# Kernel optimization log

Hardware: AMD Instinct MI355X
Metric: run time of the kernel (lower is better)

The kernel has to match this reference:

```python
import jax, jax.numpy as jnp
import numpy as np
from jax import lax

N = 1024          # proposals per image
C = 32            # num classes (incl. background at index 0)
FEAT = 4096       # box-head feature dim
NDIM = 3          # voxel boxes, zyxzyx
SCORE_THRESH = 0.05
NMS_THR = 0.5
PER_CLS_TOPN = 300
DET_PER_IMG = 100
W_CTR = jnp.array([10.0, 10.0, 10.0])
W_SIZE = jnp.array([5.0, 5.0, 5.0])
BBOX_XFORM_CLIP = float(np.log(1000.0 / 16.0))
IMG_SIZE = jnp.array([96.0, 320.0, 320.0])


def decode_boxes(reg, boxes):
    # reg: [N, C, 6] (dz,dy,dx,dsz,dsy,dsx); boxes: [N, 6] zyxzyx, TO_REMOVE=1 convention
    sizes = boxes[:, 3:] - boxes[:, :3] + 1.0            # [N,3]
    ctrs = boxes[:, :3] + 0.5 * sizes                    # [N,3]
    d_ctr = reg[..., :3] / W_CTR                         # [N,C,3]
    d_size = jnp.minimum(reg[..., 3:] / W_SIZE, BBOX_XFORM_CLIP)
    pred_ctr = d_ctr * sizes[:, None, :] + ctrs[:, None, :]
    pred_size = jnp.exp(d_size) * sizes[:, None, :]
    mins = pred_ctr - 0.5 * pred_size
    maxs = pred_ctr + 0.5 * pred_size - 1.0
    return jnp.concatenate([mins, maxs], axis=-1)        # [N,C,6]


def iou3d(b):
    # b: [M,6] zyxzyx -> [M,M] IoU (volume with +1 convention)
    lt = jnp.maximum(b[:, None, :3], b[None, :, :3])
    rb = jnp.minimum(b[:, None, 3:], b[None, :, 3:])
    whd = jnp.clip(rb - lt + 1.0, 0.0)
    inter = whd.prod(-1)
    vol = jnp.clip(b[:, 3:] - b[:, :3] + 1.0, 0.0).prod(-1)
    return inter / (vol[:, None] + vol[None, :] - inter + 1e-12)


def per_class_nms(boxes_j, scores_j):
    # boxes_j: [N,6], scores_j: [N] (softmax probs for one foreground class)
    valid = scores_j > SCORE_THRESH
    s = jnp.where(valid, scores_j, -1.0)
    order = jnp.argsort(-s)                # sorted indices (score desc), padded at end
    sb = boxes_j[order]
    ss = s[order]
    sv = valid[order]
    M = iou3d(sb)
    idx = jnp.arange(N)

    def body(i, keep):
        sup = (M[i] > NMS_THR) & (idx > i) & keep[i] & sv[i]
        return keep & ~sup

    keep = lax.fori_loop(0, N, body, sv)
    keep = keep & sv
    rank = jnp.cumsum(keep.astype(jnp.int32)) - 1
    keep = keep & (rank < PER_CLS_TOPN)
    return sb, jnp.where(keep, ss, -1.0), order, keep


def _forward(features, class_logits, box_regression, proposal_boxes):
    probs = jax.nn.softmax(class_logits, axis=-1)        # [N,C]
    reg = box_regression.reshape(N, C, 2 * NDIM)
    boxes = decode_boxes(reg, proposal_boxes)            # [N,C,6]
    # clip_to_image (remove_empty=False)
    lim = IMG_SIZE - 1.0
    boxes = jnp.concatenate([jnp.clip(boxes[..., :3], 0.0, lim),
                             jnp.clip(boxes[..., 3:], 0.0, lim)], axis=-1)
    cls_boxes = jnp.swapaxes(boxes, 0, 1)[1:]            # [C-1,N,6] skip background
    cls_scores = probs.T[1:]                             # [C-1,N]
    sb, ss, order, keep = jax.vmap(per_class_nms)(cls_boxes, cls_scores)
    all_scores = ss.reshape(-1)                          # [(C-1)*N], -1 where dropped
    all_boxes = sb.reshape(-1, 2 * NDIM)
    all_orig = order.reshape(-1)
    all_labels = jnp.broadcast_to(jnp.arange(1, C)[:, None], (C - 1, N)).reshape(-1)
    # global sort by score desc, keep top detections_per_img
    top_s, top_i = lax.top_k(all_scores, DET_PER_IMG)
    valid = top_s > 0.0
    orig = all_orig[top_i]                               # original proposal index
    feats = jnp.where(valid[:, None], features[orig], 0.0)
    pboxes = jnp.where(valid[:, None], all_boxes[top_i], 0.0)
    pscores = jnp.where(valid, top_s, 0.0)
    plabels = jnp.where(valid, all_labels[top_i], 0)
    return feats, pboxes, pscores, plabels, valid


def setup_inputs() -> dict:
    key = jax.random.key(0)
    k1, k2, k3, k4, k5 = jax.random.split(key, 5)
    features = jax.random.normal(k1, (N, FEAT), dtype=jnp.float32)
    class_logits = 2.0 * jax.random.normal(k2, (N, C), dtype=jnp.float32)
    box_regression = jax.random.normal(k3, (N, C * 2 * NDIM), dtype=jnp.float32)
    img = np.array([96.0, 320.0, 320.0], dtype=np.float32)
    mins = jax.random.uniform(k4, (N, NDIM), dtype=jnp.float32) * (img * 0.75)
    ext = jax.random.uniform(k5, (N, NDIM), dtype=jnp.float32) * (img * 0.25) + 1.0
    proposal_boxes = jnp.concatenate([mins, mins + ext - 1.0], axis=-1)
    return {"features": features, "class_logits": class_logits,
            "box_regression": box_regression, "proposal_boxes": proposal_boxes}


def reference(features, class_logits, box_regression, proposal_boxes):
    return _forward(features, class_logits, box_regression, proposal_boxes)
```

## Files before the change

kernel.cpp:

```cpp
#include <hip/hip_runtime.h>
#include <math.h>

#define NPROP 1024
#define NCLS 32
#define FEATD 4096
#define SCORE_THRESH 0.05f
#define NMS_THR 0.5f
#define DET_PER_IMG 100
#define CLS_STRIDE 128
#define BBOX_CLIP 4.135166556742356f

__device__ __forceinline__ unsigned long long u64max(unsigned long long a,
                                                     unsigned long long b) {
    return a > b ? a : b;
}

__device__ __forceinline__ unsigned flip_f32(float f) {
    unsigned u = __float_as_uint(f);
    return u ^ ((unsigned)(((int)u) >> 31) | 0x80000000u);
}
__device__ __forceinline__ float unflip_f32(unsigned u) {
    u = (u & 0x80000000u) ? (u ^ 0x80000000u) : ~u;
    return __uint_as_float(u);
}

__device__ __forceinline__ unsigned long long shfl_xor_u64(unsigned long long v,
                                                           int mask) {
    return (unsigned long long)__shfl_xor((long long)v, mask);
}

__device__ __forceinline__ void decode_box(const float* __restrict__ prop,
                                           const float* __restrict__ reg,
                                           int n, int cls, float b[6]) {
    const float lim[3] = {95.0f, 319.0f, 319.0f};
    const float* r6 = reg + n * (NCLS * 6) + cls * 6;
#pragma unroll
    for (int d = 0; d < 3; ++d) {
        float lo = prop[n * 6 + d];
        float hi = prop[n * 6 + 3 + d];
        float sz = __fadd_rn(__fsub_rn(hi, lo), 1.0f);
        float ct = __fadd_rn(lo, __fmul_rn(0.5f, sz));
        float dc = r6[d] / 10.0f;
        float ds = fminf(r6[3 + d] / 5.0f, BBOX_CLIP);
        float pc = __fadd_rn(__fmul_rn(dc, sz), ct);
        float ps = __fmul_rn(expf(ds), sz);
        float hps = __fmul_rn(0.5f, ps);
        float mn = __fsub_rn(pc, hps);
        float mx = __fsub_rn(__fadd_rn(pc, hps), 1.0f);
        b[d]     = fminf(fmaxf(mn, 0.0f), lim[d]);
        b[3 + d] = fminf(fmaxf(mx, 0.0f), lim[d]);
    }
}

__global__ __launch_bounds__(1024) void nms_kernel(const float* __restrict__ logits,
                                                   const float* __restrict__ reg,
                                                   const float* __restrict__ prop,
                                                   float* __restrict__ scores_c,
                                                   int* __restrict__ orig_c,
                                                   int* __restrict__ counts) {
    const int cls = blockIdx.x + 1;
    const int tid = threadIdx.x;
    const int lane = tid & 63, wid = tid >> 6;

    __shared__ unsigned long long kbuf[2][NPROP];
    __shared__ float sb[NPROP][6];
    __shared__ float vols[NPROP];
    __shared__ unsigned long long keepw[16];
    __shared__ int   wtot[16];
    __shared__ int   kept_cum[2];

    const float* lrow = logits + tid * NCLS;
    float4 q[8];
#pragma unroll
    for (int r = 0; r < 8; ++r) q[r] = ((const float4*)lrow)[r];
    float m = -1e30f;
#pragma unroll
    for (int r = 0; r < 8; ++r)
        m = fmaxf(m, fmaxf(fmaxf(q[r].x, q[r].y), fmaxf(q[r].z, q[r].w)));
    float ssum = 0.0f;
#pragma unroll
    for (int r = 0; r < 8; ++r) {
        ssum += expf(q[r].x - m);
        ssum += expf(q[r].y - m);
        ssum += expf(q[r].z - m);
        ssum += expf(q[r].w - m);
    }
    float xc = lrow[cls];
    float p = expf(xc - m) / ssum;
    float sv0 = (p > SCORE_THRESH) ? p : -1.0f;

    unsigned long long key =
        ((unsigned long long)flip_f32(sv0) << 32) | (unsigned)~tid;
    int pb = 0;
    for (int k = 2; k <= NPROP; k <<= 1) {
        for (int j = k >> 1; j > 0; j >>= 1) {
            unsigned long long pk;
            if (j >= 64) {
                kbuf[pb][tid] = key;
                __syncthreads();
                pk = kbuf[pb][tid ^ j];
                pb ^= 1;
            } else {
                pk = shfl_xor_u64(key, j);
            }
            bool lower = (tid & j) == 0;
            bool desc  = (tid & k) == 0;
            bool want_max = (lower == desc);
            bool pk_gt = pk > key;
            key = (want_max == pk_gt) ? pk : key;
        }
    }
    float sv = unflip_f32((unsigned)(key >> 32));
    int o = (int)(~(unsigned)key);

    float myb[6];
    decode_box(prop, reg, o, cls, myb);
#pragma unroll
    for (int d = 0; d < 6; ++d) sb[tid][d] = myb[d];
    float myvol = 1.0f;
#pragma unroll
    for (int d = 0; d < 3; ++d)
        myvol *= fmaxf(myb[3 + d] - myb[d] + 1.0f, 0.0f);
    vols[tid] = myvol;

    int mykeep = (sv > SCORE_THRESH) ? 1 : 0;
    unsigned long long m0 = __ballot(mykeep);
    if (lane == 0) keepw[wid] = m0;
    if (tid == 0) { kept_cum[0] = 0; kept_cum[1] = 0; }
    __syncthreads();

    for (int w = 0; w < 16; ++w) {
        if (kept_cum[w & 1] >= DET_PER_IMG) break;
        unsigned long long wk = 0;
        if (wid >= w) {
            wk = keepw[w];
            const int base = w << 6;
            if (wk) {
                float w0 = sb[base + lane][0], w1 = sb[base + lane][1];
                float w2 = sb[base + lane][2], w3 = sb[base + lane][3];
                float w4 = sb[base + lane][4], w5 = sb[base + lane][5];
                float wv = vols[base + lane];
                unsigned long long rest = wk;
                while (rest) {
                    int b = __ffsll((long long)rest) - 1;
                    rest &= rest - 1;
                    float b0 = sb[base + b][0], b1 = sb[base + b][1];
                    float b2 = sb[base + b][2], b3 = sb[base + b][3];
                    float b4 = sb[base + b][4], b5 = sb[base + b][5];
                    float bv = vols[base + b];
                    bool sup = false;
                    if (lane > b && ((wk >> lane) & 1)) {
                        float i0 = fmaxf(fminf(w3, b3) - fmaxf(w0, b0) + 1.0f, 0.0f);
                        float i1 = fmaxf(fminf(w4, b4) - fmaxf(w1, b1) + 1.0f, 0.0f);
                        float i2 = fmaxf(fminf(w5, b5) - fmaxf(w2, b2) + 1.0f, 0.0f);
                        float inter = i0 * i1 * i2;
                        sup = inter / (bv + wv - inter + 1e-12f) > NMS_THR;
                    }
                    unsigned long long supm = __ballot(sup);
                    wk &= ~supm;
                    rest &= ~supm;
                }
                if (wid == w) {
                    mykeep = (int)((wk >> lane) & 1);
                } else if (mykeep) {
                    unsigned long long t = wk;
                    while (t) {
                        int bb = __ffsll((long long)t) - 1;
                        t &= t - 1;
                        float b0 = sb[base + bb][0], b1 = sb[base + bb][1];
                        float b2 = sb[base + bb][2], b3 = sb[base + bb][3];
                        float b4 = sb[base + bb][4], b5 = sb[base + bb][5];
                        float bv = vols[base + bb];
                        float i0 = fmaxf(fminf(myb[3], b3) - fmaxf(myb[0], b0) + 1.0f, 0.0f);
                        float i1 = fmaxf(fminf(myb[4], b4) - fmaxf(myb[1], b1) + 1.0f, 0.0f);
                        float i2 = fmaxf(fminf(myb[5], b5) - fmaxf(myb[2], b2) + 1.0f, 0.0f);
                        float inter = i0 * i1 * i2;
                        if (inter / (bv + myvol - inter + 1e-12f) > NMS_THR) {
                            mykeep = 0;
                            break;
                        }
                    }
                }
            }
            if (wid == w && lane == 0)
                kept_cum[(w + 1) & 1] = kept_cum[w & 1] + __popcll(wk);
        }
        unsigned long long mm = __ballot(mykeep);
        if (lane == 0) keepw[wid] = mm;
        __syncthreads();
    }

    unsigned long long mask = __ballot(mykeep);
    int pre = __popcll(mask & ((1ull << lane) - 1ull));
    if (lane == 0) wtot[wid] = __popcll(mask);
    __syncthreads();
    int before = 0;
    for (int w = 0; w < wid; ++w) before += wtot[w];
    int rank = before + pre;

    if (mykeep && rank < DET_PER_IMG) {
        scores_c[(cls - 1) * CLS_STRIDE + rank] = sv;
        orig_c[(cls - 1) * CLS_STRIDE + rank] = o;
    }
    if (tid == 0) {
        int tot = 0;
#pragma unroll
        for (int w = 0; w < 16; ++w) tot += wtot[w];
        counts[cls - 1] = tot < DET_PER_IMG ? tot : DET_PER_IMG;
    }
}

__global__ __launch_bounds__(64) void topk_kernel(const float* __restrict__ scores_c,
                                                  const int* __restrict__ counts,
                                                  float* __restrict__ tk_score,
                                                  int* __restrict__ tk_idx) {
    const int lane = threadIdx.x;
    __shared__ float lsc[31 * CLS_STRIDE];

    const float4* src4 = (const float4*)scores_c;
    float4* dst4 = (float4*)lsc;
#pragma unroll
    for (int t = 0; t < 16; ++t) {
        int idx = t * 64 + lane;
        if (idx < (31 * CLS_STRIDE) / 4) dst4[idx] = src4[idx];
    }
    int cnt = (lane < 31) ? counts[lane] : 0;
    if (cnt > DET_PER_IMG) cnt = DET_PER_IMG;
    __syncthreads();

    unsigned long long head = 0;
    if (lane < 31 && cnt > 0) {
        unsigned u = __float_as_uint(lsc[lane * CLS_STRIDE]) | 0x80000000u;
        head = ((unsigned long long)u << 32) | (unsigned)~(lane << 7);
    }

    for (int it = 0; it < DET_PER_IMG; ++it) {
        unsigned long long wb = head;
#pragma unroll
        for (int off = 1; off < 64; off <<= 1)
            wb = u64max(wb, shfl_xor_u64(wb, off));
        if (wb == 0) {
            if (lane == 0) { tk_score[it] = -1.0f; tk_idx[it] = 0; }
            continue;
        }
        unsigned v = ~(unsigned)wb;
        if (lane == 0) {
            tk_score[it] = __uint_as_float((unsigned)(wb >> 32) & 0x7fffffffu);
            tk_idx[it] = (int)v;
        }
        int c = (int)(v >> 7), r = (int)(v & 127);
        if (lane == c) {
            int pos = r + 1;
            head = 0;
            if (pos < cnt) {
                unsigned u = __float_as_uint(lsc[lane * CLS_STRIDE + pos]) | 0x80000000u;
                head = ((unsigned long long)u << 32) | (unsigned)~((lane << 7) | pos);
            }
        }
    }
}

__global__ void gather_kernel(const float* __restrict__ features,
                              const float* __restrict__ prop,
                              const float* __restrict__ reg,
                              const int* __restrict__ orig_c,
                              const float* __restrict__ tk_score,
                              const int* __restrict__ tk_idx,
                              float* __restrict__ out) {
    const int k = blockIdx.x;
    const int tid = threadIdx.x;
    float sc = tk_score[k];
    int flat = tk_idx[k];
    bool valid = sc > 0.0f;
    int cls = (flat >> 7) + 1;
    int orig = valid ? orig_c[flat] : 0;

    const float4* src = (const float4*)(features + (size_t)orig * FEATD);
    float4* dstf = (float4*)(out + (size_t)k * FEATD);
    const float4 z4 = make_float4(0.f, 0.f, 0.f, 0.f);
#pragma unroll
    for (int t = 0; t < 4; ++t) {
        int idx = tid + t * 256;
        dstf[idx] = valid ? src[idx] : z4;
    }

    const size_t boxOff = (size_t)DET_PER_IMG * FEATD;
    if (tid == 0) {
        float bb[6];
        decode_box(prop, reg, orig, cls, bb);
#pragma unroll
        for (int d = 0; d < 6; ++d)
            out[boxOff + k * 6 + d] = valid ? bb[d] : 0.0f;
    }
    if (tid == 1) out[boxOff + 600 + k] = valid ? sc : 0.0f;
    if (tid == 2) out[boxOff + 700 + k] = valid ? (float)cls : 0.0f;
    if (tid == 3) out[boxOff + 800 + k] = valid ? 1.0f : 0.0f;
}

extern "C" void kernel_launch(void* const* d_in, const int* in_sizes, int n_in,
                              void* d_out, int out_size, void* d_ws, size_t ws_size,
                              hipStream_t stream) {
    (void)in_sizes; (void)n_in; (void)out_size; (void)ws_size;
    const float* features = (const float*)d_in[0];
    const float* logits   = (const float*)d_in[1];
    const float* reg      = (const float*)d_in[2];
    const float* prop     = (const float*)d_in[3];
    float* out = (float*)d_out;

    float* scores_c = (float*)d_ws;
    int*   orig_c   = (int*)(scores_c + 31 * CLS_STRIDE);
    int*   counts   = (int*)(orig_c + 31 * CLS_STRIDE);
    float* tk_score = (float*)(counts + 32);
    int*   tk_idx   = (int*)(tk_score + DET_PER_IMG);

    nms_kernel<<<NCLS - 1, 1024, 0, stream>>>(logits, reg, prop,
                                              scores_c, orig_c, counts);
    topk_kernel<<<1, 64, 0, stream>>>(scores_c, counts, tk_score, tk_idx);
    gather_kernel<<<DET_PER_IMG, 256, 0, stream>>>(
        features, prop, reg, orig_c, tk_score, tk_idx, out);
}
```

Measured before the change: 172.7 us.

## Restructure NMS rounds with readlane broadcasts and bound rounds by valid count

The blocked NMS loop is reorganized. Only the owning wavefront resolves intra-block suppression, using readlane broadcasts from registers instead of shared-memory reads. It then publishes a keep mask, and the other waves check their candidates against it after a barrier. The number of rounds is capped by the count of valid boxes so empty trailing blocks are skipped, at the cost of an extra barrier per round. In the top-k kernel the reduction is narrowed to 32 lanes and the next head is prefetched to shorten the serial dependency per iteration.

```diff
diff --git a/kernel.cpp b/kernel.cpp
--- a/kernel.cpp
+++ b/kernel.cpp
@@ -27,6 +27,14 @@
 __device__ __forceinline__ unsigned long long shfl_xor_u64(unsigned long long v,
                                                            int mask) {
     return (unsigned long long)__shfl_xor((long long)v, mask);
+}
+__device__ __forceinline__ unsigned long long shfl_xor_u64_w32(unsigned long long v,
+                                                               int mask) {
+    return (unsigned long long)__shfl_xor((long long)v, mask, 32);
+}
+
+__device__ __forceinline__ float readlane_f32(float v, int l) {
+    return __uint_as_float((unsigned)__builtin_amdgcn_readlane(__float_as_uint(v), l));
 }
 
 __device__ __forceinline__ void decode_box(const float* __restrict__ prop,
@@ -63,10 +71,10 @@
     const int lane = tid & 63, wid = tid >> 6;
 
     __shared__ unsigned long long kbuf[2][NPROP];
-    __shared__ float sb[NPROP][6];
-    __shared__ float vols[NPROP];
+    __shared__ float sbv[NPROP][7];
     __shared__ unsigned long long keepw[16];
     __shared__ int   wtot[16];
+    __shared__ int   wvalid[16];
     __shared__ int   kept_cum[2];
 
     const float* lrow = logits + tid * NCLS;
@@ -116,77 +124,85 @@
     float myb[6];
     decode_box(prop, reg, o, cls, myb);
 #pragma unroll
-    for (int d = 0; d < 6; ++d) sb[tid][d] = myb[d];
+    for (int d = 0; d < 6; ++d) sbv[tid][d] = myb[d];
     float myvol = 1.0f;
 #pragma unroll
     for (int d = 0; d < 3; ++d)
         myvol *= fmaxf(myb[3 + d] - myb[d] + 1.0f, 0.0f);
-    vols[tid] = myvol;
+    sbv[tid][6] = myvol;
 
     int mykeep = (sv > SCORE_THRESH) ? 1 : 0;
-    unsigned long long m0 = __ballot(mykeep);
-    if (lane == 0) keepw[wid] = m0;
+    unsigned long long vb = __ballot(mykeep);
+    if (lane == 0) wvalid[wid] = __popcll(vb);
     if (tid == 0) { kept_cum[0] = 0; kept_cum[1] = 0; }
     __syncthreads();
 
-    for (int w = 0; w < 16; ++w) {
+    int nv = 0;
+#pragma unroll
+    for (int w = 0; w < 16; ++w) nv += wvalid[w];
+    int nrounds = (nv + 63) >> 6;
+
+    for (int w = 0; w < nrounds; ++w) {
         if (kept_cum[w & 1] >= DET_PER_IMG) break;
-        unsigned long long wk = 0;
-        if (wid >= w) {
-            wk = keepw[w];
-            const int base = w << 6;
-            if (wk) {
-                float w0 = sb[base + lane][0], w1 = sb[base + lane][1];
-                float w2 = sb[base + lane][2], w3 = sb[base + lane][3];
-                float w4 = sb[base + lane][4], w5 = sb[base + lane][5];
-                float wv = vols[base + lane];
-                unsigned long long rest = wk;
-                while (rest) {
-                    int b = __ffsll((long long)rest) - 1;
-                    rest &= rest - 1;
-                    float b0 = sb[base + b][0], b1 = sb[base + b][1];
-                    float b2 = sb[base + b][2], b3 = sb[base + b][3];
-                    float b4 = sb[base + b][4], b5 = sb[base + b][5];
-                    float bv = vols[base + b];
-                    bool sup = false;
-                    if (lane > b && ((wk >> lane) & 1)) {
-                        float i0 = fmaxf(fminf(w3, b3) - fmaxf(w0, b0) + 1.0f, 0.0f);
-                        float i1 = fmaxf(fminf(w4, b4) - fmaxf(w1, b1) + 1.0f, 0.0f);
-                        float i2 = fmaxf(fminf(w5, b5) - fmaxf(w2, b2) + 1.0f, 0.0f);
-                        float inter = i0 * i1 * i2;
-                        sup = inter / (bv + wv - inter + 1e-12f) > NMS_THR;
-                    }
-                    unsigned long long supm = __ballot(sup);
-                    wk &= ~supm;
-                    rest &= ~supm;
+        const int base = w << 6;
+
+        if (wid == w) {
+            unsigned long long wk = __ballot(mykeep);
+            unsigned long long rest = wk;
+            while (rest) {
+                int b = __ffsll((long long)rest) - 1;
+                rest &= rest - 1;
+                float b0 = readlane_f32(myb[0], b), b1 = readlane_f32(myb[1], b);
+                float b2 = readlane_f32(myb[2], b), b3 = readlane_f32(myb[3], b);
+                float b4 = readlane_f32(myb[4], b), b5 = readlane_f32(myb[5], b);
+                float bv = readlane_f32(myvol, b);
+                bool sup = false;
+                if (lane > b && ((wk >> lane) & 1)) {
+                    float i0 = fmaxf(fminf(myb[3], b3) - fmaxf(myb[0], b0) + 1.0f, 0.0f);
+                    float i1 = fmaxf(fminf(myb[4], b4) - fmaxf(myb[1], b1) + 1.0f, 0.0f);
+                    float i2 = fmaxf(fminf(myb[5], b5) - fmaxf(myb[2], b2) + 1.0f, 0.0f);
+                    float inter = i0 * i1 * i2;
+                    sup = inter / (bv + myvol - inter + 1e-12f) > NMS_THR;
                 }
-                if (wid == w) {
-                    mykeep = (int)((wk >> lane) & 1);
-                } else if (mykeep) {
-                    unsigned long long t = wk;
-                    while (t) {
-                        int bb = __ffsll((long long)t) - 1;
-                        t &= t - 1;
-                        float b0 = sb[base + bb][0], b1 = sb[base + bb][1];
-                        float b2 = sb[base + bb][2], b3 = sb[base + bb][3];
-                        float b4 = sb[base + bb][4], b5 = sb[base + bb][5];
-                        float bv = vols[base + bb];
-                        float i0 = fmaxf(fminf(myb[3], b3) - fmaxf(myb[0], b0) + 1.0f, 0.0f);
-                        float i1 = fmaxf(fminf(myb[4], b4) - fmaxf(myb[1], b1) + 1.0f, 0.0f);
-                        float i2 = fmaxf(fminf(myb[5], b5) - fmaxf(myb[2], b2) + 1.0f, 0.0f);
-                        float inter = i0 * i1 * i2;
-                        if (inter / (bv + myvol - inter + 1e-12f) > NMS_THR) {
-                            mykeep = 0;
-                            break;
-                        }
+                unsigned long long sm = __ballot(sup);
+                wk &= ~sm;
+                rest &= ~sm;
+            }
+            mykeep = (int)((wk >> lane) & 1);
+            if (lane == 0) {
+                keepw[w] = wk;
+                kept_cum[(w + 1) & 1] = kept_cum[w & 1] + __popcll(wk);
+            }
+        }
+        __syncthreads();
+
+        unsigned long long wkf = keepw[w];
+        bool anyk = __ballot(mykeep) != 0;
+        if (wid > w && anyk && wkf) {
+            float r0 = sbv[base + lane][0], r1 = sbv[base + lane][1];
+            float r2 = sbv[base + lane][2], r3 = sbv[base + lane][3];
+            float r4 = sbv[base + lane][4], r5 = sbv[base + lane][5];
+            float rv = sbv[base + lane][6];
+            if (mykeep) {
+                unsigned long long t = wkf;
+                while (t) {
+                    int bb = __ffsll((long long)t) - 1;
+                    t &= t - 1;
+                    float b0 = readlane_f32(r0, bb), b1 = readlane_f32(r1, bb);
+                    float b2 = readlane_f32(r2, bb), b3 = readlane_f32(r3, bb);
+                    float b4 = readlane_f32(r4, bb), b5 = readlane_f32(r5, bb);
+                    float bv = readlane_f32(rv, bb);
+                    float i0 = fmaxf(fminf(myb[3], b3) - fmaxf(myb[0], b0) + 1.0f, 0.0f);
+                    float i1 = fmaxf(fminf(myb[4], b4) - fmaxf(myb[1], b1) + 1.0f, 0.0f);
+                    float i2 = fmaxf(fminf(myb[5], b5) - fmaxf(myb[2], b2) + 1.0f, 0.0f);
+                    float inter = i0 * i1 * i2;
+                    if (inter / (bv + myvol - inter + 1e-12f) > NMS_THR) {
+                        mykeep = 0;
+                        break;
                     }
                 }
             }
-            if (wid == w && lane == 0)
-                kept_cum[(w + 1) & 1] = kept_cum[w & 1] + __popcll(wk);
-        }
-        unsigned long long mm = __ballot(mykeep);
-        if (lane == 0) keepw[wid] = mm;
+        }
         __syncthreads();
     }
 
@@ -228,17 +244,24 @@
     if (cnt > DET_PER_IMG) cnt = DET_PER_IMG;
     __syncthreads();
 
-    unsigned long long head = 0;
-    if (lane < 31 && cnt > 0) {
-        unsigned u = __float_as_uint(lsc[lane * CLS_STRIDE]) | 0x80000000u;
-        head = ((unsigned long long)u << 32) | (unsigned)~(lane << 7);
+    int pos = 0;
+    unsigned long long head = 0, nxt = 0;
+    if (lane < 31) {
+        if (cnt > 0) {
+            unsigned u = __float_as_uint(lsc[lane * CLS_STRIDE]) | 0x80000000u;
+            head = ((unsigned long long)u << 32) | (unsigned)~(lane << 7);
+        }
+        if (cnt > 1) {
+            unsigned u = __float_as_uint(lsc[lane * CLS_STRIDE + 1]) | 0x80000000u;
+            nxt = ((unsigned long long)u << 32) | (unsigned)~((lane << 7) | 1);
+        }
     }
 
     for (int it = 0; it < DET_PER_IMG; ++it) {
         unsigned long long wb = head;
 #pragma unroll
-        for (int off = 1; off < 64; off <<= 1)
-            wb = u64max(wb, shfl_xor_u64(wb, off));
+        for (int off = 1; off < 32; off <<= 1)
+            wb = u64max(wb, shfl_xor_u64_w32(wb, off));
         if (wb == 0) {
             if (lane == 0) { tk_score[it] = -1.0f; tk_idx[it] = 0; }
             continue;
@@ -248,13 +271,15 @@
             tk_score[it] = __uint_as_float((unsigned)(wb >> 32) & 0x7fffffffu);
             tk_idx[it] = (int)v;
         }
-        int c = (int)(v >> 7), r = (int)(v & 127);
+        int c = (int)(v >> 7);
         if (lane == c) {
-            int pos = r + 1;
-            head = 0;
-            if (pos < cnt) {
-                unsigned u = __float_as_uint(lsc[lane * CLS_STRIDE + pos]) | 0x80000000u;
-                head = ((unsigned long long)u << 32) | (unsigned)~((lane << 7) | pos);
+            ++pos;
+            head = nxt;
+            int p2 = pos + 1;
+            nxt = 0;
+            if (p2 < cnt) {
+                unsigned u = __float_as_uint(lsc[lane * CLS_STRIDE + p2]) | 0x80000000u;
+                nxt = ((unsigned long long)u << 32) | (unsigned)~((lane << 7) | p2);
             }
         }
     }
```

Result: no change. 169.7 us (-1.7%).
